# Optimization experiments

Hardware: AMD Instinct MI355X
Metric: run time of the kernel (lower is better)

## Reference

```python
import jax, jax.numpy as jnp
import numpy as np

B, LA, LS, C, H = 4, 1536, 512, 256, 4
DK = C // H
NEG = -jnp.inf


def _pad(lengths, maxlen):
    # True where padded (idx >= length)
    return jnp.arange(maxlen)[None, :] >= lengths[:, None]


def build_mask(l_v, l_s, ilens, ylens):
    """Additive float mask [B, l_v+l_s, l_v+l_s] with 0 / -inf, matching
    generate_multi_modal_mask_new."""
    b = ilens.shape[0]
    i = jnp.arange(l_s)
    causal = jnp.where(i[:, None] >= i[None, :], 0.0, NEG)            # [l_s, l_s]
    tgt_pad = _pad(ylens, l_s)                                        # [b, l_s]
    mask_s_s = jnp.where(tgt_pad[:, None, :], NEG, causal[None])      # [b, l_s, l_s]
    src_row = jnp.where(_pad(ilens, l_v), NEG, 0.0)                   # [b, l_v]
    mask_v_v = jnp.broadcast_to(src_row[:, None, :], (b, l_v, l_v))
    mask_s_v = jnp.broadcast_to(src_row[:, None, :], (b, l_s, l_v))
    mask_v_s = jnp.full((b, l_v, l_s), NEG, dtype=jnp.float32)
    top = jnp.concatenate([mask_v_v, mask_v_s], axis=2)
    bot = jnp.concatenate([mask_s_v, mask_s_s], axis=2)
    return jnp.concatenate([top, bot], axis=1)


def setup_inputs() -> dict:
    key = jax.random.key(0)
    ks = jax.random.split(key, 12)
    scale = 1.0 / np.sqrt(C)
    return {
        "audio_encoder_out": jax.random.normal(ks[0], (B, LA, C), jnp.float32),
        "text_encoder_out": jax.random.normal(ks[1], (B, LS, C), jnp.float32),
        "speech_length": jax.random.randint(ks[2], (B,), 1, LA),
        "text_length": jax.random.randint(ks[3], (B,), 1, LS),
        "Wq": jax.random.normal(ks[4], (C, C), jnp.float32) * scale,
        "bq": jax.random.normal(ks[5], (C,), jnp.float32) * scale,
        "Wk": jax.random.normal(ks[6], (C, C), jnp.float32) * scale,
        "bk": jax.random.normal(ks[7], (C,), jnp.float32) * scale,
        "Wv": jax.random.normal(ks[8], (C, C), jnp.float32) * scale,
        "bv": jax.random.normal(ks[9], (C,), jnp.float32) * scale,
        "Wo": jax.random.normal(ks[10], (C, C), jnp.float32) * scale,
        "bo": jax.random.normal(ks[11], (C,), jnp.float32) * scale,
    }


def reference(audio_encoder_out, text_encoder_out, speech_length, text_length,
              Wq, bq, Wk, bk, Wv, bv, Wo, bo):
    b, l_a, c = audio_encoder_out.shape
    l_s = text_encoder_out.shape[1]
    x = jnp.concatenate([audio_encoder_out, text_encoder_out], axis=1)  # [B, L, C]
    L = l_a + l_s

    def heads(W, bias):
        return (x @ W.T + bias).reshape(b, L, H, DK).transpose(0, 2, 1, 3)  # [B,H,L,DK]

    q, k, v = heads(Wq, bq), heads(Wk, bk), heads(Wv, bv)
    scores = jnp.einsum("bhqd,bhkd->bhqk", q, k) / np.float32(np.sqrt(DK))

    amask = build_mask(l_a, l_s, speech_length, text_length)  # additive [B,L,L]
    # Faithful to torch: mask.eq(0) positions (additive-0) are filled with -inf,
    # then zeroed in attn (the module's inverted masking behavior).
    eq0 = (amask == 0.0)[:, None, :, :]                       # [B,1,L,L]
    scores = jnp.where(eq0, NEG, scores)
    attn = jax.nn.softmax(scores, axis=-1)
    attn = jnp.where(eq0, 0.0, attn)                          # (dropout = identity, eval)
    out = jnp.einsum("bhqk,bhkd->bhqd", attn, v)
    out = out.transpose(0, 2, 1, 3).reshape(b, L, H * DK)
    return out @ Wo.T + bo
```

## Files before the change

kernel.cpp:

```cpp
#include <hip/hip_runtime.h>
#include <hip/hip_bf16.h>
#include <math.h>

#define LA 1536
#define LS 512
#define LT 2048
#define CC 256
#define NH 4
#define DKH 64
#define NB 4
#define NT (LT / 64)

typedef _Float16 f16;
typedef __attribute__((ext_vector_type(8))) _Float16 f16x8;
typedef __attribute__((ext_vector_type(4))) _Float16 f16x4;
typedef __attribute__((ext_vector_type(4))) float f32x4;

__device__ inline f16x8 cvt8(const float4 a, const float4 b) {
    f16x8 h;
    h[0] = (_Float16)a.x; h[1] = (_Float16)a.y; h[2] = (_Float16)a.z; h[3] = (_Float16)a.w;
    h[4] = (_Float16)b.x; h[5] = (_Float16)b.y; h[6] = (_Float16)b.z; h[7] = (_Float16)b.w;
    return h;
}

__global__ __launch_bounds__(256) void qkv_mfma(
    const float* __restrict__ audio, const float* __restrict__ text,
    const float* __restrict__ Wq, const float* __restrict__ bq,
    const float* __restrict__ Wk, const float* __restrict__ bk,
    const float* __restrict__ Wv, const float* __restrict__ bv,
    f16* __restrict__ Qh, f16* __restrict__ Kh, f16* __restrict__ Vth)
{
    __shared__ f16 As[128 * 64];
    __shared__ f16 Bs[64 * 64];

    const int tid = threadIdx.x;
    const int w = tid >> 6, l = tid & 63;
    const int g = l >> 4, r = l & 15;

    const int m0 = blockIdx.x * 128;
    const int n0 = blockIdx.y * 64;
    const int mat = n0 >> 8;
    const int ch0 = n0 & 255;

    const float* W    = (mat == 0) ? Wq : (mat == 1) ? Wk : Wv;
    const float* bias = (mat == 0) ? bq : (mat == 1) ? bk : bv;

    const int b  = m0 >> 11;
    const int l0 = m0 & 2047;

    f32x4 acc[2][4] = {};

    for (int k0 = 0; k0 < CC; k0 += 64) {
        #pragma unroll
        for (int m = 0; m < 4; ++m) {
            const int idx = m * 256 + tid;
            const int row = idx >> 3, c = idx & 7;
            const int lrow = l0 + row;
            const float* src = (lrow < LA)
                ? (audio + ((size_t)b * LA + lrow) * CC + k0 + c * 8)
                : (text  + ((size_t)b * LS + (lrow - LA)) * CC + k0 + c * 8);
            const float4 x0 = *(const float4*)src;
            const float4 x1 = *(const float4*)(src + 4);
            *(f16x8*)(As + row * 64 + ((c ^ (row & 7)) << 3)) = cvt8(x0, x1);
        }
        #pragma unroll
        for (int m = 0; m < 2; ++m) {
            const int idx = m * 256 + tid;
            const int row = idx >> 3, c = idx & 7;
            const float* src = W + (size_t)(ch0 + row) * CC + k0 + c * 8;
            const float4 x0 = *(const float4*)src;
            const float4 x1 = *(const float4*)(src + 4);
            *(f16x8*)(Bs + row * 64 + ((c ^ (row & 7)) << 3)) = cvt8(x0, x1);
        }
        __syncthreads();
        #pragma unroll
        for (int kc = 0; kc < 2; ++kc) {
            f16x8 af[2];
            #pragma unroll
            for (int i = 0; i < 2; ++i) {
                const int row = w * 32 + i * 16 + r;
                const int c = kc * 4 + g;
                af[i] = *(const f16x8*)(As + row * 64 + ((c ^ (row & 7)) << 3));
            }
            f16x8 bf[4];
            #pragma unroll
            for (int j = 0; j < 4; ++j) {
                const int row = j * 16 + r;
                const int c = kc * 4 + g;
                bf[j] = *(const f16x8*)(Bs + row * 64 + ((c ^ (row & 7)) << 3));
            }
            #pragma unroll
            for (int i = 0; i < 2; ++i)
                #pragma unroll
                for (int j = 0; j < 4; ++j)
                    acc[i][j] = __builtin_amdgcn_mfma_f32_16x16x32_f16(af[i], bf[j], acc[i][j], 0, 0, 0);
        }
        __syncthreads();
    }

    float bcol[4];
    #pragma unroll
    for (int j = 0; j < 4; ++j) bcol[j] = bias[ch0 + j * 16 + r];

    if (mat <= 1) {
        f16* Out = (mat == 0) ? Qh : Kh;
        #pragma unroll
        for (int i = 0; i < 2; ++i)
            #pragma unroll
            for (int e = 0; e < 4; ++e) {
                const int m = m0 + w * 32 + i * 16 + g * 4 + e;
                #pragma unroll
                for (int j = 0; j < 4; ++j)
                    Out[(size_t)m * CC + ch0 + j * 16 + r] = (_Float16)(acc[i][j][e] + bcol[j]);
            }
    } else {
        #pragma unroll
        for (int i = 0; i < 2; ++i)
            #pragma unroll
            for (int e = 0; e < 4; ++e) {
                const int m = m0 + w * 32 + i * 16 + g * 4 + e;
                const int b2 = m >> 11, ll = m & 2047;
                #pragma unroll
                for (int j = 0; j < 4; ++j) {
                    const int n = ch0 + j * 16 + r;
                    const int hh = n >> 6, dd = n & 63;
                    Vth[((size_t)(b2 * NH + hh) * DKH + dd) * LT + ll] =
                        (_Float16)(acc[i][j][e] + bcol[j]);
                }
            }
    }
}

__global__ __launch_bounds__(256) void attn_f16(
    const f16* __restrict__ Q, const f16* __restrict__ K,
    const f16* __restrict__ Vt,
    const int* __restrict__ slen, const int* __restrict__ tlen,
    f16* __restrict__ AO)
{
    __shared__ f16 Ks[2][4096];
    __shared__ f16 Vts[2][4096];
    __shared__ f16 Ps[4][16 * 72];

    const int tid = threadIdx.x;
    const int w = tid >> 6;
    const int l = tid & 63;
    const int g = l >> 4;
    const int r = l & 15;

    const int q0 = blockIdx.x * 64;
    const int h  = blockIdx.y;
    const int b  = blockIdx.z;

    const int ilen = slen[b];
    const int kcap = LA + tlen[b];
    const int nskip = ilen >> 6;

    const int qrow = q0 + 16 * w + r;

    f16x8 qf[2];
    #pragma unroll
    for (int ch = 0; ch < 2; ++ch) {
        f16x8 q8 = *(const f16x8*)(Q + ((size_t)(b * LT) + qrow) * CC + h * DKH + ch * 32 + g * 8);
        #pragma unroll
        for (int e = 0; e < 8; ++e) q8[e] = q8[e] * (_Float16)0.125f;
        qf[ch] = q8;
    }

    const int srow0 = tid >> 3,            sc0 = tid & 7;
    const int srow1 = (256 + tid) >> 3,    sc1 = tid & 7;
    const int sdst0 = srow0 * 64 + ((sc0 ^ (srow0 & 7)) << 3);
    const int sdst1 = srow1 * 64 + ((sc1 ^ (srow1 & 7)) << 3);

    {
        const int k0 = nskip * 64;
        *(f16x8*)(Ks[0] + sdst0) = *(const f16x8*)(K + ((size_t)(b * LT) + k0 + srow0) * CC + h * DKH + sc0 * 8);
        *(f16x8*)(Vts[0] + sdst0) = *(const f16x8*)(Vt + ((size_t)((b * NH + h) * DKH) + srow0) * LT + k0 + sc0 * 8);
        *(f16x8*)(Ks[0] + sdst1) = *(const f16x8*)(K + ((size_t)(b * LT) + k0 + srow1) * CC + h * DKH + sc1 * 8);
        *(f16x8*)(Vts[0] + sdst1) = *(const f16x8*)(Vt + ((size_t)((b * NH + h) * DKH) + srow1) * LT + k0 + sc1 * 8);
    }
    __syncthreads();

    float m_run = -INFINITY, l_run = 0.0f;
    f32x4 o[4] = {};

    int cur = 0;
    for (int kt = nskip; kt < NT; ++kt) {
        const int k0 = kt * 64;
        const bool have_next = (kt + 1 < NT);

        f16x8 kr0, vr0, kr1, vr1;
        if (have_next) {
            const int kn = k0 + 64;
            kr0 = *(const f16x8*)(K + ((size_t)(b * LT) + kn + srow0) * CC + h * DKH + sc0 * 8);
            vr0 = *(const f16x8*)(Vt + ((size_t)((b * NH + h) * DKH) + srow0) * LT + kn + sc0 * 8);
            kr1 = *(const f16x8*)(K + ((size_t)(b * LT) + kn + srow1) * CC + h * DKH + sc1 * 8);
            vr1 = *(const f16x8*)(Vt + ((size_t)((b * NH + h) * DKH) + srow1) * LT + kn + sc1 * 8);
        }

        f32x4 sacc[4] = {};
        #pragma unroll
        for (int s = 0; s < 4; ++s) {
            const int row = 16 * s + r;
            #pragma unroll
            for (int ch = 0; ch < 2; ++ch) {
                const f16x8 a = *(const f16x8*)(Ks[cur] + row * 64 + ((((ch * 4 + g) ^ (row & 7)) & 7) << 3));
                sacc[s] = __builtin_amdgcn_mfma_f32_16x16x32_f16(a, qf[ch], sacc[s], 0, 0, 0);
            }
        }

        const int mode = (kt < LA / 64) ? ((k0 >= ilen) ? 0 : 1)
                                        : ((q0 < LA) ? 0 : 2);
        float sv[16];
        if (mode == 0) {
            #pragma unroll
            for (int s = 0; s < 4; ++s)
                #pragma unroll
                for (int e = 0; e < 4; ++e) sv[s * 4 + e] = sacc[s][e];
        } else if (mode == 1) {
            #pragma unroll
            for (int s = 0; s < 4; ++s)
                #pragma unroll
                for (int e = 0; e < 4; ++e) {
                    const int kk = k0 + 16 * s + 4 * g + e;
                    sv[s * 4 + e] = (kk >= ilen) ? sacc[s][e] : -INFINITY;
                }
        } else {
            #pragma unroll
            for (int s = 0; s < 4; ++s)
                #pragma unroll
                for (int e = 0; e < 4; ++e) {
                    const int kk = k0 + 16 * s + 4 * g + e;
                    sv[s * 4 + e] = (kk > qrow || kk >= kcap) ? sacc[s][e] : -INFINITY;
                }
        }

        float mloc = -INFINITY;
        #pragma unroll
        for (int u = 0; u < 16; ++u) mloc = fmaxf(mloc, sv[u]);
        mloc = fmaxf(mloc, __shfl_xor(mloc, 16));
        mloc = fmaxf(mloc, __shfl_xor(mloc, 32));
        const float m_new = fmaxf(m_run, mloc);

        float ssum = 0.0f;
        f16x4 ph[4];
        #pragma unroll
        for (int s = 0; s < 4; ++s)
            #pragma unroll
            for (int e = 0; e < 4; ++e) {
                const float p = __expf(sv[s * 4 + e] - m_new);
                ph[s][e] = (_Float16)p;
                ssum += p;
            }
        ssum += __shfl_xor(ssum, 16);
        ssum += __shfl_xor(ssum, 32);
        const float sc = __expf(m_run - m_new);
        l_run = l_run * sc + ssum;
        m_run = m_new;

        #pragma unroll
        for (int s = 0; s < 4; ++s)
            *(f16x4*)(&Ps[w][0] + r * 72 + 16 * s + 4 * g) = ph[s];

        #pragma unroll
        for (int e = 0; e < 4; ++e) {
            const float scr = __shfl(sc, 4 * g + e);
            #pragma unroll
            for (int dsb = 0; dsb < 4; ++dsb) o[dsb][e] *= scr;
        }

        #pragma unroll
        for (int ch = 0; ch < 2; ++ch) {
            const f16x8 a = *(const f16x8*)(&Ps[w][0] + r * 72 + ch * 32 + g * 8);
            #pragma unroll
            for (int dsb = 0; dsb < 4; ++dsb) {
                const int vrow = 16 * dsb + r;
                const f16x8 bf = *(const f16x8*)(Vts[cur] + vrow * 64 + ((((ch * 4 + g) ^ (vrow & 7)) & 7) << 3));
                o[dsb] = __builtin_amdgcn_mfma_f32_16x16x32_f16(a, bf, o[dsb], 0, 0, 0);
            }
        }

        if (have_next) {
            const int nxt = cur ^ 1;
            *(f16x8*)(Ks[nxt] + sdst0) = kr0;
            *(f16x8*)(Vts[nxt] + sdst0) = vr0;
            *(f16x8*)(Ks[nxt] + sdst1) = kr1;
            *(f16x8*)(Vts[nxt] + sdst1) = vr1;
        }
        __syncthreads();
        cur ^= 1;
    }

    const float linv = 1.0f / l_run;
    #pragma unroll
    for (int e = 0; e < 4; ++e) {
        const float inv = __shfl(linv, 4 * g + e);
        const int qq = q0 + 16 * w + 4 * g + e;
        #pragma unroll
        for (int dsb = 0; dsb < 4; ++dsb)
            AO[((size_t)(b * LT) + qq) * CC + h * DKH + 16 * dsb + r] =
                (_Float16)(o[dsb][e] * inv);
    }
}

__global__ __launch_bounds__(256) void out_mfma(
    const f16* __restrict__ X, const float* __restrict__ Wo,
    const float* __restrict__ bo, float* __restrict__ Out)
{
    __shared__ f16 As[128 * 64];
    __shared__ f16 Bs[64 * 64];

    const int tid = threadIdx.x;
    const int w = tid >> 6, l = tid & 63;
    const int g = l >> 4, r = l & 15;

    const int m0 = blockIdx.x * 128;
    const int n0 = blockIdx.y * 64;

    f32x4 acc[2][4] = {};

    for (int k0 = 0; k0 < CC; k0 += 64) {
        #pragma unroll
        for (int m = 0; m < 4; ++m) {
            const int idx = m * 256 + tid;
            const int row = idx >> 3, c = idx & 7;
            *(f16x8*)(As + row * 64 + ((c ^ (row & 7)) << 3)) =
                *(const f16x8*)(X + (size_t)(m0 + row) * CC + k0 + c * 8);
        }
        #pragma unroll
        for (int m = 0; m < 2; ++m) {
            const int idx = m * 256 + tid;
            const int row = idx >> 3, c = idx & 7;
            const float* src = Wo + (size_t)(n0 + row) * CC + k0 + c * 8;
            const float4 x0 = *(const float4*)src;
            const float4 x1 = *(const float4*)(src + 4);
            *(f16x8*)(Bs + row * 64 + ((c ^ (row & 7)) << 3)) = cvt8(x0, x1);
        }
        __syncthreads();
        #pragma unroll
        for (int kc = 0; kc < 2; ++kc) {
            f16x8 af[2];
            #pragma unroll
            for (int i = 0; i < 2; ++i) {
                const int row = w * 32 + i * 16 + r;
                const int c = kc * 4 + g;
                af[i] = *(const f16x8*)(As + row * 64 + ((c ^ (row & 7)) << 3));
            }
            f16x8 bf[4];
            #pragma unroll
            for (int j = 0; j < 4; ++j) {
                const int row = j * 16 + r;
                const int c = kc * 4 + g;
                bf[j] = *(const f16x8*)(Bs + row * 64 + ((c ^ (row & 7)) << 3));
            }
            #pragma unroll
            for (int i = 0; i < 2; ++i)
                #pragma unroll
                for (int j = 0; j < 4; ++j)
                    acc[i][j] = __builtin_amdgcn_mfma_f32_16x16x32_f16(af[i], bf[j], acc[i][j], 0, 0, 0);
        }
        __syncthreads();
    }

    float bcol[4];
    #pragma unroll
    for (int j = 0; j < 4; ++j) bcol[j] = bo[n0 + j * 16 + r];

    #pragma unroll
    for (int i = 0; i < 2; ++i)
        #pragma unroll
        for (int e = 0; e < 4; ++e) {
            const int m = m0 + w * 32 + i * 16 + g * 4 + e;
            #pragma unroll
            for (int j = 0; j < 4; ++j)
                Out[(size_t)m * CC + n0 + j * 16 + r] = acc[i][j][e] + bcol[j];
        }
}

extern "C" void kernel_launch(void* const* d_in, const int* in_sizes, int n_in,
                              void* d_out, int out_size, void* d_ws, size_t ws_size,
                              hipStream_t stream)
{
    const float* audio = (const float*)d_in[0];
    const float* text  = (const float*)d_in[1];
    const int*   slen  = (const int*)d_in[2];
    const int*   tlen  = (const int*)d_in[3];
    const float* Wq = (const float*)d_in[4];
    const float* bq = (const float*)d_in[5];
    const float* Wk = (const float*)d_in[6];
    const float* bk = (const float*)d_in[7];
    const float* Wv = (const float*)d_in[8];
    const float* bv = (const float*)d_in[9];
    const float* Wo = (const float*)d_in[10];
    const float* bo = (const float*)d_in[11];
    float* out = (float*)d_out;

    const size_t SZ = (size_t)NB * LT * CC;
    f16* Qh  = (f16*)d_ws;
    f16* Kh  = Qh + SZ;
    f16* Vth = Kh + SZ;
    f16* AOh = Vth + SZ;

    qkv_mfma<<<dim3(64, 12), 256, 0, stream>>>(audio, text, Wq, bq, Wk, bk, Wv, bv,
                                               Qh, Kh, Vth);
    attn_f16<<<dim3(LT / 64, NH, NB), 256, 0, stream>>>(Qh, Kh, Vth, slen, tlen, AOh);
    out_mfma<<<dim3(64, 4), 256, 0, stream>>>(AOh, Wo, bo, out);
}
```

Before: 54.07 us.

## Split attention KV loop across two warp groups and stage V transpose through LDS

The attention kernel now launches 512 threads, and two 4-wave groups each process alternate KV tiles with their own LDS buffers. The partial softmax states (max, sum and output) are merged through shared memory at the end. It also skips text tiles that are fully masked for text query rows, and it writes the transposed V in the QKV kernel through an LDS staging buffer so global stores are coalesced. The intent is to raise per-block parallelism, skip useless tiles and fix strided V stores. The cost is extra LDS, a merge step, and prefetch that now goes through registers with two barriers per iteration.

```diff
diff --git a/kernel.cpp b/kernel.cpp
--- a/kernel.cpp
+++ b/kernel.cpp
@@ -10,6 +10,7 @@
 #define DKH 64
 #define NB 4
 #define NT (LT / 64)
+#define NTA (LA / 64)
 
 typedef _Float16 f16;
 typedef __attribute__((ext_vector_type(8))) _Float16 f16x8;
@@ -30,8 +31,9 @@
     const float* __restrict__ Wv, const float* __restrict__ bv,
     f16* __restrict__ Qh, f16* __restrict__ Kh, f16* __restrict__ Vth)
 {
-    __shared__ f16 As[128 * 64];
-    __shared__ f16 Bs[64 * 64];
+    __shared__ f16 smem[128 * 64 + 64 * 64];
+    f16* As = smem;
+    f16* Bs = smem + 128 * 64;
 
     const int tid = threadIdx.x;
     const int w = tid >> 6, l = tid & 63;
@@ -114,24 +116,31 @@
                     Out[(size_t)m * CC + ch0 + j * 16 + r] = (_Float16)(acc[i][j][e] + bcol[j]);
             }
     } else {
+        f16* Ts = smem;
         #pragma unroll
         for (int i = 0; i < 2; ++i)
             #pragma unroll
             for (int e = 0; e < 4; ++e) {
-                const int m = m0 + w * 32 + i * 16 + g * 4 + e;
-                const int b2 = m >> 11, ll = m & 2047;
-                #pragma unroll
-                for (int j = 0; j < 4; ++j) {
-                    const int n = ch0 + j * 16 + r;
-                    const int hh = n >> 6, dd = n & 63;
-                    Vth[((size_t)(b2 * NH + hh) * DKH + dd) * LT + ll] =
-                        (_Float16)(acc[i][j][e] + bcol[j]);
-                }
-            }
+                const int ml = w * 32 + i * 16 + g * 4 + e;
+                #pragma unroll
+                for (int j = 0; j < 4; ++j)
+                    Ts[(j * 16 + r) * 136 + ml] = (_Float16)(acc[i][j][e] + bcol[j]);
+            }
+        __syncthreads();
+        const int b2 = m0 >> 11, l0m = m0 & 2047;
+        #pragma unroll
+        for (int u = 0; u < 4; ++u) {
+            const int idx = u * 256 + tid;
+            const int nl = idx >> 4, mc = idx & 15;
+            const f16x8 vv = *(const f16x8*)(Ts + nl * 136 + mc * 8);
+            const int nglob = ch0 + nl;
+            const int hh = nglob >> 6, dd = nglob & 63;
+            *(f16x8*)(Vth + ((size_t)((b2 * NH + hh) * DKH + dd)) * LT + l0m + mc * 8) = vv;
+        }
     }
 }
 
-__global__ __launch_bounds__(256) void attn_f16(
+__global__ __launch_bounds__(512) void attn_f16(
     const f16* __restrict__ Q, const f16* __restrict__ K,
     const f16* __restrict__ Vt,
     const int* __restrict__ slen, const int* __restrict__ tlen,
@@ -139,13 +148,15 @@
 {
     __shared__ f16 Ks[2][4096];
     __shared__ f16 Vts[2][4096];
-    __shared__ f16 Ps[4][16 * 72];
+    __shared__ f16 Ps[8][16 * 72];
+    __shared__ float Oc[4][1024];
+    __shared__ float ML[2][64][2];
 
     const int tid = threadIdx.x;
-    const int w = tid >> 6;
-    const int l = tid & 63;
-    const int g = l >> 4;
-    const int r = l & 15;
+    const int w = tid >> 6, l = tid & 63;
+    const int gid = w >> 2, wg = w & 3;
+    const int g = l >> 4, r = l & 15;
+    const int tg = tid & 255;
 
     const int q0 = blockIdx.x * 64;
     const int h  = blockIdx.y;
@@ -154,8 +165,17 @@
     const int ilen = slen[b];
     const int kcap = LA + tlen[b];
     const int nskip = ilen >> 6;
-
-    const int qrow = q0 + 16 * w + r;
+    int ntskip = 0;
+    if (q0 >= LA) {
+        const int skipmax = min(q0 - 63, kcap - 64);
+        const int d = skipmax - LA;
+        ntskip = (d < 0) ? 0 : ((d >> 6) + 1);
+    }
+    const int nAudio = NTA - nskip;
+    const int nProc  = nAudio + (NT - NTA) - ntskip;
+    const int nIter  = (nProc + 1) >> 1;
+
+    const int qrow = q0 + 16 * wg + r;
 
     f16x8 qf[2];
     #pragma unroll
@@ -166,140 +186,165 @@
         qf[ch] = q8;
     }
 
-    const int srow0 = tid >> 3,            sc0 = tid & 7;
-    const int srow1 = (256 + tid) >> 3,    sc1 = tid & 7;
-    const int sdst0 = srow0 * 64 + ((sc0 ^ (srow0 & 7)) << 3);
-    const int sdst1 = srow1 * 64 + ((sc1 ^ (srow1 & 7)) << 3);
+    const int srow0 = tg >> 3, scc = tg & 7;
+    const int srow1 = srow0 + 32;
+    const int sdst0 = srow0 * 64 + ((scc ^ (srow0 & 7)) << 3);
+    const int sdst1 = srow1 * 64 + ((scc ^ (srow1 & 7)) << 3);
+
+    #define TILE_OF(p) ((p) < nAudio ? (nskip + (p)) : (NTA + ntskip + ((p) - nAudio)))
 
     {
-        const int k0 = nskip * 64;
-        *(f16x8*)(Ks[0] + sdst0) = *(const f16x8*)(K + ((size_t)(b * LT) + k0 + srow0) * CC + h * DKH + sc0 * 8);
-        *(f16x8*)(Vts[0] + sdst0) = *(const f16x8*)(Vt + ((size_t)((b * NH + h) * DKH) + srow0) * LT + k0 + sc0 * 8);
-        *(f16x8*)(Ks[0] + sdst1) = *(const f16x8*)(K + ((size_t)(b * LT) + k0 + srow1) * CC + h * DKH + sc1 * 8);
-        *(f16x8*)(Vts[0] + sdst1) = *(const f16x8*)(Vt + ((size_t)((b * NH + h) * DKH) + srow1) * LT + k0 + sc1 * 8);
+        const int k0 = TILE_OF(gid) * 64;
+        *(f16x8*)(Ks[gid] + sdst0)  = *(const f16x8*)(K  + ((size_t)(b * LT) + k0 + srow0) * CC + h * DKH + scc * 8);
+        *(f16x8*)(Vts[gid] + sdst0) = *(const f16x8*)(Vt + ((size_t)((b * NH + h) * DKH) + srow0) * LT + k0 + scc * 8);
+        *(f16x8*)(Ks[gid] + sdst1)  = *(const f16x8*)(K  + ((size_t)(b * LT) + k0 + srow1) * CC + h * DKH + scc * 8);
+        *(f16x8*)(Vts[gid] + sdst1) = *(const f16x8*)(Vt + ((size_t)((b * NH + h) * DKH) + srow1) * LT + k0 + scc * 8);
+    }
+
+    float m_run = -1e30f, l_run = 0.0f;
+    f32x4 o[4] = {};
+
+    for (int i = 0; i < nIter; ++i) {
+        __syncthreads();
+        const int pcur = 2 * i + gid;
+        const bool curV = pcur < nProc;
+        const bool nxtV = (pcur + 2) < nProc;
+
+        f16x8 kr0, vr0, kr1, vr1;
+        if (nxtV) {
+            const int kn = TILE_OF(pcur + 2) * 64;
+            kr0 = *(const f16x8*)(K  + ((size_t)(b * LT) + kn + srow0) * CC + h * DKH + scc * 8);
+            vr0 = *(const f16x8*)(Vt + ((size_t)((b * NH + h) * DKH) + srow0) * LT + kn + scc * 8);
+            kr1 = *(const f16x8*)(K  + ((size_t)(b * LT) + kn + srow1) * CC + h * DKH + scc * 8);
+            vr1 = *(const f16x8*)(Vt + ((size_t)((b * NH + h) * DKH) + srow1) * LT + kn + scc * 8);
+        }
+
+        if (curV) {
+            const int kt = TILE_OF(pcur);
+            const int k0 = kt * 64;
+
+            f32x4 sacc[4] = {};
+            #pragma unroll
+            for (int s = 0; s < 4; ++s) {
+                const int row = 16 * s + r;
+                #pragma unroll
+                for (int ch = 0; ch < 2; ++ch) {
+                    const f16x8 a = *(const f16x8*)(Ks[gid] + row * 64 + ((((ch * 4 + g) ^ (row & 7)) & 7) << 3));
+                    sacc[s] = __builtin_amdgcn_mfma_f32_16x16x32_f16(a, qf[ch], sacc[s], 0, 0, 0);
+                }
+            }
+
+            const int mode = (kt < NTA) ? ((k0 >= ilen) ? 0 : 1)
+                                        : ((q0 < LA) ? 0 : 2);
+            float sv[16];
+            if (mode == 0) {
+                #pragma unroll
+                for (int s = 0; s < 4; ++s)
+                    #pragma unroll
+                    for (int e = 0; e < 4; ++e) sv[s * 4 + e] = sacc[s][e];
+            } else if (mode == 1) {
+                #pragma unroll
+                for (int s = 0; s < 4; ++s)
+                    #pragma unroll
+                    for (int e = 0; e < 4; ++e) {
+                        const int kk = k0 + 16 * s + 4 * g + e;
+                        sv[s * 4 + e] = (kk >= ilen) ? sacc[s][e] : -INFINITY;
+                    }
+            } else {
+                #pragma unroll
+                for (int s = 0; s < 4; ++s)
+                    #pragma unroll
+                    for (int e = 0; e < 4; ++e) {
+                        const int kk = k0 + 16 * s + 4 * g + e;
+                        sv[s * 4 + e] = (kk > qrow || kk >= kcap) ? sacc[s][e] : -INFINITY;
+                    }
+            }
+
+            float mloc = -1e30f;
+            #pragma unroll
+            for (int u = 0; u < 16; ++u) mloc = fmaxf(mloc, sv[u]);
+            mloc = fmaxf(mloc, __shfl_xor(mloc, 16));
+            mloc = fmaxf(mloc, __shfl_xor(mloc, 32));
+            const float m_new = fmaxf(m_run, mloc);
+
+            float ssum = 0.0f;
+            f16x4 ph[4];
+            #pragma unroll
+            for (int s = 0; s < 4; ++s)
+                #pragma unroll
+                for (int e = 0; e < 4; ++e) {
+                    const float p = __expf(sv[s * 4 + e] - m_new);
+                    ph[s][e] = (_Float16)p;
+                    ssum += p;
+                }
+            ssum += __shfl_xor(ssum, 16);
+            ssum += __shfl_xor(ssum, 32);
+            const float sc = __expf(m_run - m_new);
+            l_run = l_run * sc + ssum;
+            m_run = m_new;
+
+            #pragma unroll
+            for (int s = 0; s < 4; ++s)
+                *(f16x4*)(&Ps[w][0] + r * 72 + 16 * s + 4 * g) = ph[s];
+
+            #pragma unroll
+            for (int e = 0; e < 4; ++e) {
+                const float scr = __shfl(sc, 4 * g + e);
+                #pragma unroll
+                for (int dsb = 0; dsb < 4; ++dsb) o[dsb][e] *= scr;
+            }
+
+            #pragma unroll
+            for (int ch = 0; ch < 2; ++ch) {
+                const f16x8 a = *(const f16x8*)(&Ps[w][0] + r * 72 + ch * 32 + g * 8);
+                #pragma unroll
+                for (int dsb = 0; dsb < 4; ++dsb) {
+                    const int vrow = 16 * dsb + r;
+                    const f16x8 bf = *(const f16x8*)(Vts[gid] + vrow * 64 + ((((ch * 4 + g) ^ (vrow & 7)) & 7) << 3));
+                    o[dsb] = __builtin_amdgcn_mfma_f32_16x16x32_f16(a, bf, o[dsb], 0, 0, 0);
+                }
+            }
+        }
+
+        __syncthreads();
+        if (nxtV) {
+            *(f16x8*)(Ks[gid] + sdst0)  = kr0;
+            *(f16x8*)(Vts[gid] + sdst0) = vr0;
+            *(f16x8*)(Ks[gid] + sdst1)  = kr1;
+            *(f16x8*)(Vts[gid] + sdst1) = vr1;
+        }
+    }
+
+    if (g == 0) {
+        ML[gid][16 * wg + r][0] = m_run;
+        ML[gid][16 * wg + r][1] = l_run;
+    }
+    if (gid == 1) {
+        #pragma unroll
+        for (int dsb = 0; dsb < 4; ++dsb)
+            *(f32x4*)&Oc[wg][dsb * 256 + (g * 16 + r) * 4] = o[dsb];
     }
     __syncthreads();
 
-    float m_run = -INFINITY, l_run = 0.0f;
-    f32x4 o[4] = {};
-
-    int cur = 0;
-    for (int kt = nskip; kt < NT; ++kt) {
-        const int k0 = kt * 64;
-        const bool have_next = (kt + 1 < NT);
-
-        f16x8 kr0, vr0, kr1, vr1;
-        if (have_next) {
-            const int kn = k0 + 64;
-            kr0 = *(const f16x8*)(K + ((size_t)(b * LT) + kn + srow0) * CC + h * DKH + sc0 * 8);
-            vr0 = *(const f16x8*)(Vt + ((size_t)((b * NH + h) * DKH) + srow0) * LT + kn + sc0 * 8);
-            kr1 = *(const f16x8*)(K + ((size_t)(b * LT) + kn + srow1) * CC + h * DKH + sc1 * 8);
-            vr1 = *(const f16x8*)(Vt + ((size_t)((b * NH + h) * DKH) + srow1) * LT + kn + sc1 * 8);
-        }
-
-        f32x4 sacc[4] = {};
-        #pragma unroll
-        for (int s = 0; s < 4; ++s) {
-            const int row = 16 * s + r;
-            #pragma unroll
-            for (int ch = 0; ch < 2; ++ch) {
-                const f16x8 a = *(const f16x8*)(Ks[cur] + row * 64 + ((((ch * 4 + g) ^ (row & 7)) & 7) << 3));
-                sacc[s] = __builtin_amdgcn_mfma_f32_16x16x32_f16(a, qf[ch], sacc[s], 0, 0, 0);
-            }
-        }
-
-        const int mode = (kt < LA / 64) ? ((k0 >= ilen) ? 0 : 1)
-                                        : ((q0 < LA) ? 0 : 2);
-        float sv[16];
-        if (mode == 0) {
-            #pragma unroll
-            for (int s = 0; s < 4; ++s)
-                #pragma unroll
-                for (int e = 0; e < 4; ++e) sv[s * 4 + e] = sacc[s][e];
-        } else if (mode == 1) {
-            #pragma unroll
-            for (int s = 0; s < 4; ++s)
-                #pragma unroll
-                for (int e = 0; e < 4; ++e) {
-                    const int kk = k0 + 16 * s + 4 * g + e;
-                    sv[s * 4 + e] = (kk >= ilen) ? sacc[s][e] : -INFINITY;
-                }
-        } else {
-            #pragma unroll
-            for (int s = 0; s < 4; ++s)
-                #pragma unroll
-                for (int e = 0; e < 4; ++e) {
-                    const int kk = k0 + 16 * s + 4 * g + e;
-                    sv[s * 4 + e] = (kk > qrow || kk >= kcap) ? sacc[s][e] : -INFINITY;
-                }
-        }
-
-        float mloc = -INFINITY;
-        #pragma unroll
-        for (int u = 0; u < 16; ++u) mloc = fmaxf(mloc, sv[u]);
-        mloc = fmaxf(mloc, __shfl_xor(mloc, 16));
-        mloc = fmaxf(mloc, __shfl_xor(mloc, 32));
-        const float m_new = fmaxf(m_run, mloc);
-
-        float ssum = 0.0f;
-        f16x4 ph[4];
-        #pragma unroll
-        for (int s = 0; s < 4; ++s)
-            #pragma unroll
-            for (int e = 0; e < 4; ++e) {
-                const float p = __expf(sv[s * 4 + e] - m_new);
-                ph[s][e] = (_Float16)p;
-                ssum += p;
-            }
-        ssum += __shfl_xor(ssum, 16);
-        ssum += __shfl_xor(ssum, 32);
-        const float sc = __expf(m_run - m_new);
-        l_run = l_run * sc + ssum;
-        m_run = m_new;
-
-        #pragma unroll
-        for (int s = 0; s < 4; ++s)
-            *(f16x4*)(&Ps[w][0] + r * 72 + 16 * s + 4 * g) = ph[s];
-
+    if (gid == 0) {
         #pragma unroll
         for (int e = 0; e < 4; ++e) {
-            const float scr = __shfl(sc, 4 * g + e);
-            #pragma unroll
-            for (int dsb = 0; dsb < 4; ++dsb) o[dsb][e] *= scr;
-        }
-
-        #pragma unroll
-        for (int ch = 0; ch < 2; ++ch) {
-            const f16x8 a = *(const f16x8*)(&Ps[w][0] + r * 72 + ch * 32 + g * 8);
+            const int qloc = 16 * wg + 4 * g + e;
+            const float m0v = ML[0][qloc][0], l0v = ML[0][qloc][1];
+            const float m1v = ML[1][qloc][0], l1v = ML[1][qloc][1];
+            const float mt = fmaxf(m0v, m1v);
+            const float c0 = __expf(m0v - mt);
+            const float c1 = __expf(m1v - mt);
+            const float inv = 1.0f / (l0v * c0 + l1v * c1);
+            const int qq = q0 + qloc;
             #pragma unroll
             for (int dsb = 0; dsb < 4; ++dsb) {
-                const int vrow = 16 * dsb + r;
-                const f16x8 bf = *(const f16x8*)(Vts[cur] + vrow * 64 + ((((ch * 4 + g) ^ (vrow & 7)) & 7) << 3));
-                o[dsb] = __builtin_amdgcn_mfma_f32_16x16x32_f16(a, bf, o[dsb], 0, 0, 0);
-            }
-        }
-
-        if (have_next) {
-            const int nxt = cur ^ 1;
-            *(f16x8*)(Ks[nxt] + sdst0) = kr0;
-            *(f16x8*)(Vts[nxt] + sdst0) = vr0;
-            *(f16x8*)(Ks[nxt] + sdst1) = kr1;
-            *(f16x8*)(Vts[nxt] + sdst1) = vr1;
-        }
-        __syncthreads();
-        cur ^= 1;
-    }
-
-    const float linv = 1.0f / l_run;
-    #pragma unroll
-    for (int e = 0; e < 4; ++e) {
-        const float inv = __shfl(linv, 4 * g + e);
-        const int qq = q0 + 16 * w + 4 * g + e;
-        #pragma unroll
-        for (int dsb = 0; dsb < 4; ++dsb)
-            AO[((size_t)(b * LT) + qq) * CC + h * DKH + 16 * dsb + r] =
-                (_Float16)(o[dsb][e] * inv);
-    }
+                const float of = (o[dsb][e] * c0 + Oc[wg][dsb * 256 + (g * 16 + r) * 4 + e] * c1) * inv;
+                AO[((size_t)(b * LT) + qq) * CC + h * DKH + 16 * dsb + r] = (_Float16)of;
+            }
+        }
+    }
+    #undef TILE_OF
 }
 
 __global__ __launch_bounds__(256) void out_mfma(
@@ -402,6 +447,6 @@
 
     qkv_mfma<<<dim3(64, 12), 256, 0, stream>>>(audio, text, Wq, bq, Wk, bk, Wv, bv,
                                                Qh, Kh, Vth);
-    attn_f16<<<dim3(LT / 64, NH, NB), 256, 0, stream>>>(Qh, Kh, Vth, slen, tlen, AOh);
+    attn_f16<<<dim3(LT / 64, NH, NB), 512, 0, stream>>>(Qh, Kh, Vth, slen, tlen, AOh);
     out_mfma<<<dim3(64, 4), 256, 0, stream>>>(AOh, Wo, bo, out);
 }
```

Result: faster. 49.30 us (-8.8%).
